# Optimization experiments

Measured on AMD Instinct MI355X. Metric: run time of the kernel, lower is better.

The kernel has to match this reference:

```python
import jax, jax.numpy as jnp
import numpy as np


def setup_inputs() -> dict:
    key = jax.random.key(0)
    kx, kw = jax.random.split(key)
    x = jax.random.normal(kx, (8192, 4096), dtype=jnp.float32)
    # weights initialized ~ N(0, 0.1) as in RandomNormal(stddev=0.1)
    w = jax.random.normal(kw, (4096, 4096), dtype=jnp.float32) * 0.1
    return {"x": x, "w": w}


def reference(x, w):
    # BinaryDense: sign-binarize both activations and weights, then matmul.
    x_bin = jnp.sign(x)  # [N, d_in], values in {-1, 0, +1}
    w_bin = jnp.sign(w)  # [d_in, units]
    return jnp.matmul(x_bin, w_bin)  # [N, units]
```

## Files before the change

### kernel.cpp

```cpp
#include <hip/hip_runtime.h>


#define M_DIM 8192
#define K_DIM 4096
#define N_DIM 4096
#define KB2   (K_DIM / 2)
#define HALFB 64
#define NH    (KB2 / HALFB)
#define HTILE (256 * HALFB)
#define SLOTB (2 * HTILE)

typedef int   v4i  __attribute__((ext_vector_type(4)));
typedef int   v8i  __attribute__((ext_vector_type(8)));
typedef float v16f __attribute__((ext_vector_type(16)));

__device__ __forceinline__ unsigned int nib4(float x) {
    return x > 0.0f ? 0x2u : (x < 0.0f ? 0xAu : 0x0u);
}

__global__ __launch_bounds__(256) void pack_both(const float* __restrict__ x,
                                                 unsigned short* __restrict__ xq,
                                                 const float* __restrict__ w,
                                                 unsigned char* __restrict__ wT) {
    if (blockIdx.x < 32768u) {
        size_t t = (size_t)blockIdx.x * 256 + threadIdx.x;
        float4 f = ((const float4*)x)[t];
        unsigned int v = nib4(f.x) | (nib4(f.y) << 4) | (nib4(f.z) << 8) | (nib4(f.w) << 12);
        xq[t] = (unsigned short)v;
        return;
    }
    __shared__ unsigned char sT[64][132];
    const unsigned id = blockIdx.x - 32768u;
    const int t  = threadIdx.x;
    const int n0 = (int)(id & 31) * 128;
    const int kb = (int)(id >> 5);
    const int k0 = kb * 64;

    const int cq = t & 31;
    const int r0 = t >> 5;
#pragma unroll
    for (int p = 0; p < 8; ++p) {
        int r = r0 + 8 * p;
        float4 f = *(const float4*)(w + (size_t)(k0 + r) * N_DIM + n0 + cq * 4);
        uchar4 c;
        c.x = (unsigned char)nib4(f.x);
        c.y = (unsigned char)nib4(f.y);
        c.z = (unsigned char)nib4(f.z);
        c.w = (unsigned char)nib4(f.w);
        *(uchar4*)(&sT[r][cq * 4]) = c;
    }
    __syncthreads();

    const int n  = t >> 1;
    const int kq = t & 1;
    union { unsigned char b[16]; int4 v; } u;
#pragma unroll
    for (int j = 0; j < 16; ++j) {
        unsigned lo = sT[kq * 32 + 2 * j][n];
        unsigned hi = sT[kq * 32 + 2 * j + 1][n];
        u.b[j] = (unsigned char)(lo | (hi << 4));
    }
    *(int4*)(wT + (size_t)(n0 + n) * KB2 + (size_t)kb * 32 + kq * 16) = u.v;
}

__device__ __forceinline__ v8i widen(v4i x) {
    v8i r;
    r[0] = x[0]; r[1] = x[1]; r[2] = x[2]; r[3] = x[3];
    r[4] = 0; r[5] = 0; r[6] = 0; r[7] = 0;
    return r;
}

__device__ __forceinline__ void gload16(const unsigned char* g, unsigned char* l) {
    __builtin_amdgcn_global_load_lds(
        (__attribute__((address_space(1))) void*)(void*)g,
        (__attribute__((address_space(3))) void*)l, 16, 0, 0);
}

__global__ __launch_bounds__(512, 2) void bgemm_fp4(const unsigned char* __restrict__ A,
                                                    const unsigned char* __restrict__ B,
                                                    float* __restrict__ C) {
    __shared__ __align__(16) unsigned char lds[4 * SLOTB];

    const int tid  = threadIdx.x;
    const int lane = tid & 63;
    const int wave = tid >> 6;
    const int wm   = wave >> 2;
    const int wn   = wave & 3;
    const int l31  = lane & 31;
    const int lhi  = lane >> 5;

    const int m0 = blockIdx.y * 256;
    const int n0 = blockIdx.x * 256;

    v16f acc[4][2] = {};

    const unsigned char* gAsrc[2];
    const unsigned char* gBsrc[2];
    int dstOff[2];
#pragma unroll
    for (int i = 0; i < 2; ++i) {
        int g   = i * 512 + tid;
        int q   = g >> 3;
        int t   = (g & 7) ^ (q & 7);
        int row = 2 * q + (t >> 2);
        int kc  = t & 3;
        gAsrc[i] = A + (size_t)(m0 + row) * KB2 + kc * 16;
        gBsrc[i] = B + (size_t)(n0 + row) * KB2 + kc * 16;
        dstOff[i] = g * 16;
    }

    int offA[2][4], offB[2][2];
#pragma unroll
    for (int ks = 0; ks < 2; ++ks) {
        const int kc = 2 * ks + lhi;
#pragma unroll
        for (int tm = 0; tm < 4; ++tm) {
            int r    = wm * 128 + tm * 32 + l31;
            int q    = r >> 1;
            int slot = (((r & 1) << 2) | kc) ^ (q & 7);
            offA[ks][tm] = q * 128 + slot * 16;
        }
#pragma unroll
        for (int tn = 0; tn < 2; ++tn) {
            int r    = wn * 64 + tn * 32 + l31;
            int q    = r >> 1;
            int slot = (((r & 1) << 2) | kc) ^ (q & 7);
            offB[ks][tn] = q * 128 + slot * 16;
        }
    }

    auto stage = [&](int h) {
        unsigned char* s = lds + (h & 3) * SLOTB;
        const size_t ko = (size_t)h * HALFB;
#pragma unroll
        for (int i = 0; i < 2; ++i) {
            gload16(gAsrc[i] + ko, s + dstOff[i]);
            gload16(gBsrc[i] + ko, s + HTILE + dstOff[i]);
        }
    };

    auto compute = [&](int h) {
        const unsigned char* sA = lds + (h & 3) * SLOTB;
        const unsigned char* sB = sA + HTILE;
#pragma unroll
        for (int ks = 0; ks < 2; ++ks) {
            v4i a4[4], b4[2];
#pragma unroll
            for (int tm = 0; tm < 4; ++tm) a4[tm] = *(const v4i*)(sA + offA[ks][tm]);
#pragma unroll
            for (int tn = 0; tn < 2; ++tn) b4[tn] = *(const v4i*)(sB + offB[ks][tn]);
            __builtin_amdgcn_s_setprio(1);
#pragma unroll
            for (int tm = 0; tm < 4; ++tm)
#pragma unroll
                for (int tn = 0; tn < 2; ++tn)
                    acc[tm][tn] = __builtin_amdgcn_mfma_scale_f32_32x32x64_f8f6f4(
                        widen(a4[tm]), widen(b4[tn]), acc[tm][tn],
                        4, 4,
                        0, 0x7F7F7F7F,
                        0, 0x7F7F7F7F);
            __builtin_amdgcn_s_setprio(0);
        }
    };

    stage(0); stage(1); stage(2);
    for (int h = 0; h < NH - 3; ++h) {
        asm volatile("s_waitcnt vmcnt(8)" ::: "memory");
        __builtin_amdgcn_s_barrier();
        stage(h + 3);
        compute(h);
    }
    asm volatile("s_waitcnt vmcnt(8)" ::: "memory");
    __builtin_amdgcn_s_barrier();
    compute(NH - 3);
    asm volatile("s_waitcnt vmcnt(4)" ::: "memory");
    __builtin_amdgcn_s_barrier();
    compute(NH - 2);
    asm volatile("s_waitcnt vmcnt(0)" ::: "memory");
    __builtin_amdgcn_s_barrier();
    compute(NH - 1);

#pragma unroll
    for (int tm = 0; tm < 4; ++tm) {
#pragma unroll
        for (int tn = 0; tn < 2; ++tn) {
            const int col  = n0 + wn * 64 + tn * 32 + l31;
            const int rowb = m0 + wm * 128 + tm * 32 + 4 * lhi;
#pragma unroll
            for (int r = 0; r < 16; ++r) {
                int row = rowb + (r & 3) + 8 * (r >> 2);
                __builtin_nontemporal_store(acc[tm][tn][r], &C[(size_t)row * N_DIM + col]);
            }
        }
    }
}

extern "C" void kernel_launch(void* const* d_in, const int* in_sizes, int n_in,
                              void* d_out, int out_size, void* d_ws, size_t ws_size,
                              hipStream_t stream) {
    const float* x = (const float*)d_in[0];
    const float* w = (const float*)d_in[1];
    float* out = (float*)d_out;

    unsigned char* xq = (unsigned char*)d_ws;
    unsigned char* wq = xq + (size_t)M_DIM * KB2;

    pack_both<<<dim3(32768 + 2048), dim3(256), 0, stream>>>(
        x, (unsigned short*)xq, w, wq);
    bgemm_fp4<<<dim3(N_DIM / 256, M_DIM / 256), dim3(512), 0, stream>>>(xq, wq, out);
}
```

Measured before the change: 324.6 us.

## Double-buffer LDS fragment reads across MFMAs and swizzle blocks per XCD

Restructures the main loop so LDS fragment loads for the next k-substep are issued while the current MFMA batch runs, using two register fragment sets, and moves the barrier to one per half-tile after staging. It also remaps a 1D grid so consecutive blocks on each XCD cover nearby output tiles, to improve L2 reuse of A/B. This costs extra registers for the second fragment set and a longer hand-unrolled epilogue.

After: 323.2 us. About the same (-0.5%).

```diff
diff --git a/kernel.cpp b/kernel.cpp
--- a/kernel.cpp
+++ b/kernel.cpp
@@ -76,6 +76,31 @@
         (__attribute__((address_space(3))) void*)l, 16, 0, 0);
 }
 
+#define RD_FRAGS(A4, B2, BASE, KS)                                   \
+    do {                                                             \
+        const unsigned char* sA_ = lds + (BASE);                     \
+        const unsigned char* sB_ = sA_ + HTILE;                      \
+        A4[0] = *(const v4i*)(sA_ + offA[KS][0]);                    \
+        A4[1] = *(const v4i*)(sA_ + offA[KS][1]);                    \
+        A4[2] = *(const v4i*)(sA_ + offA[KS][2]);                    \
+        A4[3] = *(const v4i*)(sA_ + offA[KS][3]);                    \
+        B2[0] = *(const v4i*)(sB_ + offB[KS][0]);                    \
+        B2[1] = *(const v4i*)(sB_ + offB[KS][1]);                    \
+    } while (0)
+
+#define MFMA8(A4, B2)                                                \
+    do {                                                             \
+        __builtin_amdgcn_s_setprio(1);                               \
+        _Pragma("unroll")                                            \
+        for (int tm_ = 0; tm_ < 4; ++tm_)                            \
+            _Pragma("unroll")                                        \
+            for (int tn_ = 0; tn_ < 2; ++tn_)                        \
+                acc[tm_][tn_] = __builtin_amdgcn_mfma_scale_f32_32x32x64_f8f6f4( \
+                    widen(A4[tm_]), widen(B2[tn_]), acc[tm_][tn_],   \
+                    4, 4, 0, 0x7F7F7F7F, 0, 0x7F7F7F7F);             \
+        __builtin_amdgcn_s_setprio(0);                               \
+    } while (0)
+
 __global__ __launch_bounds__(512, 2) void bgemm_fp4(const unsigned char* __restrict__ A,
                                                     const unsigned char* __restrict__ B,
                                                     float* __restrict__ C) {
@@ -89,8 +114,12 @@
     const int l31  = lane & 31;
     const int lhi  = lane >> 5;
 
-    const int m0 = blockIdx.y * 256;
-    const int n0 = blockIdx.x * 256;
+    const int id = (int)blockIdx.x;
+    const int sw = (id & 7) * 64 + (id >> 3);
+    const int bx = sw & 15;
+    const int by = sw >> 4;
+    const int m0 = by * 256;
+    const int n0 = bx * 256;
 
     v16f acc[4][2] = {};
 
@@ -139,46 +168,49 @@
         }
     };
 
-    auto compute = [&](int h) {
-        const unsigned char* sA = lds + (h & 3) * SLOTB;
-        const unsigned char* sB = sA + HTILE;
-#pragma unroll
-        for (int ks = 0; ks < 2; ++ks) {
-            v4i a4[4], b4[2];
-#pragma unroll
-            for (int tm = 0; tm < 4; ++tm) a4[tm] = *(const v4i*)(sA + offA[ks][tm]);
-#pragma unroll
-            for (int tn = 0; tn < 2; ++tn) b4[tn] = *(const v4i*)(sB + offB[ks][tn]);
-            __builtin_amdgcn_s_setprio(1);
-#pragma unroll
-            for (int tm = 0; tm < 4; ++tm)
-#pragma unroll
-                for (int tn = 0; tn < 2; ++tn)
-                    acc[tm][tn] = __builtin_amdgcn_mfma_scale_f32_32x32x64_f8f6f4(
-                        widen(a4[tm]), widen(b4[tn]), acc[tm][tn],
-                        4, 4,
-                        0, 0x7F7F7F7F,
-                        0, 0x7F7F7F7F);
-            __builtin_amdgcn_s_setprio(0);
-        }
-    };
+    v4i a0[4], b0[2];
+    v4i a1[4], b1[2];
 
     stage(0); stage(1); stage(2);
-    for (int h = 0; h < NH - 3; ++h) {
-        asm volatile("s_waitcnt vmcnt(8)" ::: "memory");
-        __builtin_amdgcn_s_barrier();
-        stage(h + 3);
-        compute(h);
-    }
-    asm volatile("s_waitcnt vmcnt(8)" ::: "memory");
-    __builtin_amdgcn_s_barrier();
-    compute(NH - 3);
     asm volatile("s_waitcnt vmcnt(4)" ::: "memory");
     __builtin_amdgcn_s_barrier();
-    compute(NH - 2);
-    asm volatile("s_waitcnt vmcnt(0)" ::: "memory");
-    __builtin_amdgcn_s_barrier();
-    compute(NH - 1);
+    RD_FRAGS(a0, b0, 0, 0);
+
+    for (int h = 0; h < NH - 3; ++h) {
+        const int sh  = (h & 3) * SLOTB;
+        const int sh1 = ((h + 1) & 3) * SLOTB;
+        RD_FRAGS(a1, b1, sh, 1);
+        MFMA8(a0, b0);
+        RD_FRAGS(a0, b0, sh1, 0);
+        stage(h + 3);
+        MFMA8(a1, b1);
+        asm volatile("s_waitcnt vmcnt(4)" ::: "memory");
+        __builtin_amdgcn_s_barrier();
+    }
+    {
+        const int sh  = ((NH - 3) & 3) * SLOTB;
+        const int sh1 = ((NH - 2) & 3) * SLOTB;
+        RD_FRAGS(a1, b1, sh, 1);
+        MFMA8(a0, b0);
+        RD_FRAGS(a0, b0, sh1, 0);
+        MFMA8(a1, b1);
+        asm volatile("s_waitcnt vmcnt(0)" ::: "memory");
+        __builtin_amdgcn_s_barrier();
+    }
+    {
+        const int sh  = ((NH - 2) & 3) * SLOTB;
+        const int sh1 = ((NH - 1) & 3) * SLOTB;
+        RD_FRAGS(a1, b1, sh, 1);
+        MFMA8(a0, b0);
+        RD_FRAGS(a0, b0, sh1, 0);
+        MFMA8(a1, b1);
+    }
+    {
+        const int sh = ((NH - 1) & 3) * SLOTB;
+        RD_FRAGS(a1, b1, sh, 1);
+        MFMA8(a0, b0);
+        MFMA8(a1, b1);
+    }
 
 #pragma unroll
     for (int tm = 0; tm < 4; ++tm) {
@@ -207,5 +239,5 @@
 
     pack_both<<<dim3(32768 + 2048), dim3(256), 0, stream>>>(
         x, (unsigned short*)xq, w, wq);
-    bgemm_fp4<<<dim3(N_DIM / 256, M_DIM / 256), dim3(512), 0, stream>>>(xq, wq, out);
-}
+    bgemm_fp4<<<dim3((M_DIM / 256) * (N_DIM / 256)), dim3(512), 0, stream>>>(xq, wq, out);
+}
```

## Load A fragments directly to registers with MFMA-ready pre-permuted packing

Applied to the files above, without the earlier changes.

The x-packing pass now writes activations in a layout that matches the MFMA lane pattern, so each wave can load its A operands straight from global memory into double-buffered registers without going through LDS. Only B stays staged in LDS, which halves LDS traffic and slot size. A 1D grid with an XCD-aware block swizzle is also added to improve L2 locality. The cost is more live registers and A loads that are no longer shared across waves, which can increase global/L2 traffic for the duplicated A reads.

Result: slower. 338.5 us (+4.3%).

```diff
diff --git a/kernel.cpp b/kernel.cpp
--- a/kernel.cpp
+++ b/kernel.cpp
@@ -7,8 +7,7 @@
 #define KB2   (K_DIM / 2)
 #define HALFB 64
 #define NH    (KB2 / HALFB)
-#define HTILE (256 * HALFB)
-#define SLOTB (2 * HTILE)
+#define SLOTB (256 * HALFB)
 
 typedef int   v4i  __attribute__((ext_vector_type(4)));
 typedef int   v8i  __attribute__((ext_vector_type(8)));
@@ -23,10 +22,16 @@
                                                  const float* __restrict__ w,
                                                  unsigned char* __restrict__ wT) {
     if (blockIdx.x < 32768u) {
-        size_t t = (size_t)blockIdx.x * 256 + threadIdx.x;
-        float4 f = ((const float4*)x)[t];
-        unsigned int v = nib4(f.x) | (nib4(f.y) << 4) | (nib4(f.z) << 8) | (nib4(f.w) << 12);
-        xq[t] = (unsigned short)v;
+        unsigned d   = blockIdx.x * 256 + threadIdx.x;
+        unsigned r5  = d >> 15;
+        unsigned h   = (d >> 10) & 31;
+        unsigned kc  = (d >> 8) & 3;
+        unsigned l31 = (d >> 3) & 31;
+        unsigned b2  = d & 7;
+        size_t   m   = (size_t)r5 * 32 + l31;
+        float4 f = ((const float4*)x)[m * 1024 + h * 32 + kc * 8 + b2];
+        unsigned v = nib4(f.x) | (nib4(f.y) << 4) | (nib4(f.z) << 8) | (nib4(f.w) << 12);
+        xq[d] = (unsigned short)v;
         return;
     }
     __shared__ unsigned char sT[64][132];
@@ -76,6 +81,35 @@
         (__attribute__((address_space(3))) void*)l, 16, 0, 0);
 }
 
+#define CLUSTER(AU, KS, BB)                                              \
+    do {                                                                 \
+        __builtin_amdgcn_s_setprio(1);                                   \
+        _Pragma("unroll")                                                \
+        for (int tm_ = 0; tm_ < 4; ++tm_)                                \
+            _Pragma("unroll")                                            \
+            for (int tn_ = 0; tn_ < 2; ++tn_)                            \
+                acc[tm_][tn_] = __builtin_amdgcn_mfma_scale_f32_32x32x64_f8f6f4( \
+                    widen(AU[(KS) * 4 + tm_]), widen(BB[tn_]), acc[tm_][tn_],    \
+                    4, 4, 0, 0x7F7F7F7F, 0, 0x7F7F7F7F);                 \
+        __builtin_amdgcn_s_setprio(0);                                   \
+    } while (0)
+
+#define BODY(H, AU, AF, DOA, DOS, VMC, DOBAR)                            \
+    do {                                                                 \
+        const unsigned char* sB_ = lds + ((H) & 3) * SLOTB;              \
+        v4i bb0_[2], bb1_[2];                                            \
+        bb0_[0] = *(const v4i*)(sB_ + offB[0][0]);                       \
+        bb0_[1] = *(const v4i*)(sB_ + offB[0][1]);                       \
+        if (DOA) loadA(AF, (H) + 1);                                     \
+        if (DOS) stageB((H) + 3);                                        \
+        CLUSTER(AU, 0, bb0_);                                            \
+        bb1_[0] = *(const v4i*)(sB_ + offB[1][0]);                       \
+        bb1_[1] = *(const v4i*)(sB_ + offB[1][1]);                       \
+        CLUSTER(AU, 1, bb1_);                                            \
+        asm volatile("s_waitcnt vmcnt(" #VMC ")" ::: "memory");          \
+        if (DOBAR) __builtin_amdgcn_s_barrier();                         \
+    } while (0)
+
 __global__ __launch_bounds__(512, 2) void bgemm_fp4(const unsigned char* __restrict__ A,
                                                     const unsigned char* __restrict__ B,
                                                     float* __restrict__ C) {
@@ -89,12 +123,14 @@
     const int l31  = lane & 31;
     const int lhi  = lane >> 5;
 
-    const int m0 = blockIdx.y * 256;
-    const int n0 = blockIdx.x * 256;
+    const int id = (int)blockIdx.x;
+    const int sw = (id & 7) * 64 + (id >> 3);
+    const int bx = sw & 15;
+    const int by = sw >> 4;
+    const int n0 = bx * 256;
 
     v16f acc[4][2] = {};
 
-    const unsigned char* gAsrc[2];
     const unsigned char* gBsrc[2];
     int dstOff[2];
 #pragma unroll
@@ -104,22 +140,14 @@
         int t   = (g & 7) ^ (q & 7);
         int row = 2 * q + (t >> 2);
         int kc  = t & 3;
-        gAsrc[i] = A + (size_t)(m0 + row) * KB2 + kc * 16;
         gBsrc[i] = B + (size_t)(n0 + row) * KB2 + kc * 16;
         dstOff[i] = g * 16;
     }
 
-    int offA[2][4], offB[2][2];
+    int offB[2][2];
 #pragma unroll
     for (int ks = 0; ks < 2; ++ks) {
         const int kc = 2 * ks + lhi;
-#pragma unroll
-        for (int tm = 0; tm < 4; ++tm) {
-            int r    = wm * 128 + tm * 32 + l31;
-            int q    = r >> 1;
-            int slot = (((r & 1) << 2) | kc) ^ (q & 7);
-            offA[ks][tm] = q * 128 + slot * 16;
-        }
 #pragma unroll
         for (int tn = 0; tn < 2; ++tn) {
             int r    = wn * 64 + tn * 32 + l31;
@@ -129,57 +157,43 @@
         }
     }
 
-    auto stage = [&](int h) {
+    const unsigned char* gA[4];
+#pragma unroll
+    for (int tm = 0; tm < 4; ++tm)
+        gA[tm] = A + ((size_t)(by * 8 + wm * 4 + tm) << 16) + lhi * 512 + l31 * 16;
+
+    auto stageB = [&](int h) {
         unsigned char* s = lds + (h & 3) * SLOTB;
         const size_t ko = (size_t)h * HALFB;
-#pragma unroll
-        for (int i = 0; i < 2; ++i) {
-            gload16(gAsrc[i] + ko, s + dstOff[i]);
-            gload16(gBsrc[i] + ko, s + HTILE + dstOff[i]);
+        gload16(gBsrc[0] + ko, s + dstOff[0]);
+        gload16(gBsrc[1] + ko, s + dstOff[1]);
+    };
+
+    v4i aA[8], aB[8];
+    auto loadA = [&](v4i (&R)[8], int h) {
+#pragma unroll
+        for (int tm = 0; tm < 4; ++tm) {
+            R[tm]     = *(const v4i*)(gA[tm] + (size_t)h * 2048);
+            R[4 + tm] = *(const v4i*)(gA[tm] + (size_t)h * 2048 + 1024);
         }
     };
 
-    auto compute = [&](int h) {
-        const unsigned char* sA = lds + (h & 3) * SLOTB;
-        const unsigned char* sB = sA + HTILE;
-#pragma unroll
-        for (int ks = 0; ks < 2; ++ks) {
-            v4i a4[4], b4[2];
-#pragma unroll
-            for (int tm = 0; tm < 4; ++tm) a4[tm] = *(const v4i*)(sA + offA[ks][tm]);
-#pragma unroll
-            for (int tn = 0; tn < 2; ++tn) b4[tn] = *(const v4i*)(sB + offB[ks][tn]);
-            __builtin_amdgcn_s_setprio(1);
-#pragma unroll
-            for (int tm = 0; tm < 4; ++tm)
-#pragma unroll
-                for (int tn = 0; tn < 2; ++tn)
-                    acc[tm][tn] = __builtin_amdgcn_mfma_scale_f32_32x32x64_f8f6f4(
-                        widen(a4[tm]), widen(b4[tn]), acc[tm][tn],
-                        4, 4,
-                        0, 0x7F7F7F7F,
-                        0, 0x7F7F7F7F);
-            __builtin_amdgcn_s_setprio(0);
-        }
-    };
-
-    stage(0); stage(1); stage(2);
-    for (int h = 0; h < NH - 3; ++h) {
-        asm volatile("s_waitcnt vmcnt(8)" ::: "memory");
-        __builtin_amdgcn_s_barrier();
-        stage(h + 3);
-        compute(h);
-    }
-    asm volatile("s_waitcnt vmcnt(8)" ::: "memory");
+    stageB(0); stageB(1); stageB(2);
+    loadA(aA, 0);
+    asm volatile("s_waitcnt vmcnt(12)" ::: "memory");
     __builtin_amdgcn_s_barrier();
-    compute(NH - 3);
-    asm volatile("s_waitcnt vmcnt(4)" ::: "memory");
-    __builtin_amdgcn_s_barrier();
-    compute(NH - 2);
-    asm volatile("s_waitcnt vmcnt(0)" ::: "memory");
-    __builtin_amdgcn_s_barrier();
-    compute(NH - 1);
-
+
+#pragma unroll 1
+    for (int h = 0; h < NH - 4; h += 2) {
+        BODY(h,     aA, aB, 1, 1, 12, 1);
+        BODY(h + 1, aB, aA, 1, 1, 12, 1);
+    }
+    BODY(28, aA, aB, 1, 1, 12, 1);
+    BODY(29, aB, aA, 1, 0, 10, 1);
+    BODY(30, aA, aB, 1, 0, 8, 1);
+    BODY(31, aB, aA, 0, 0, 0, 0);
+
+    const int m0 = by * 256;
 #pragma unroll
     for (int tm = 0; tm < 4; ++tm) {
 #pragma unroll
@@ -207,5 +221,5 @@
 
     pack_both<<<dim3(32768 + 2048), dim3(256), 0, stream>>>(
         x, (unsigned short*)xq, w, wq);
-    bgemm_fp4<<<dim3(N_DIM / 256, M_DIM / 256), dim3(512), 0, stream>>>(xq, wq, out);
-}
+    bgemm_fp4<<<dim3((M_DIM / 256) * (N_DIM / 256)), dim3(512), 0, stream>>>(xq, wq, out);
+}
```

## Interleave global-to-LDS loads with per-substep MFMA phases and swizzle block order

Applied to the files above, without the earlier changes.

Each K half-tile's compute is split into two phases. Each phase reads its LDS fragments, issues half of the next stage's global-to-LDS loads, synchronizes, and then runs its MFMAs, so loads are spread more evenly across the MFMA work. The launch grid becomes 1D, with block IDs remapped so that consecutive blocks are spread over the tile grid, which is meant to target L2 locality and XCD distribution. The change adds barriers per phase, which could increase synchronization stalls.

Result: no change. 325.4 us (+0.2%).

```diff
diff --git a/kernel.cpp b/kernel.cpp
--- a/kernel.cpp
+++ b/kernel.cpp
@@ -7,8 +7,8 @@
 #define KB2   (K_DIM / 2)
 #define HALFB 64
 #define NH    (KB2 / HALFB)
-#define HTILE (256 * HALFB)
-#define SLOTB (2 * HTILE)
+#define ATILE (256 * HALFB)
+#define SLOTB (2 * ATILE)
 
 typedef int   v4i  __attribute__((ext_vector_type(4)));
 typedef int   v8i  __attribute__((ext_vector_type(8)));
@@ -76,6 +76,39 @@
         (__attribute__((address_space(3))) void*)l, 16, 0, 0);
 }
 
+#define PHASE(H, KS, DOS, DOW, VMC, DOBAR)                               \
+    do {                                                                 \
+        const unsigned char* sA_ = lds + ((H) & 3) * SLOTB;              \
+        const unsigned char* sB_ = sA_ + ATILE;                          \
+        v4i a_[4], b_[2];                                                \
+        a_[0] = *(const v4i*)(sA_ + offA[KS][0]);                        \
+        a_[1] = *(const v4i*)(sA_ + offA[KS][1]);                        \
+        a_[2] = *(const v4i*)(sA_ + offA[KS][2]);                        \
+        a_[3] = *(const v4i*)(sA_ + offA[KS][3]);                        \
+        b_[0] = *(const v4i*)(sB_ + offB[KS][0]);                        \
+        b_[1] = *(const v4i*)(sB_ + offB[KS][1]);                        \
+        if (DOS) {                                                       \
+            unsigned char* st_ = lds + (((H) + 3) & 3) * SLOTB;          \
+            const size_t ko_ = (size_t)((H) + 3) * HALFB;                \
+            gload16(gAsrc[KS] + ko_, st_ + dstOff[KS]);                  \
+            gload16(gBsrc[KS] + ko_, st_ + ATILE + dstOff[KS]);          \
+        }                                                                \
+        __builtin_amdgcn_s_barrier();                                    \
+        asm volatile("s_waitcnt lgkmcnt(0)" ::: "memory");               \
+        __builtin_amdgcn_sched_barrier(0);                               \
+        __builtin_amdgcn_s_setprio(1);                                   \
+        _Pragma("unroll")                                                \
+        for (int tm_ = 0; tm_ < 4; ++tm_)                                \
+            _Pragma("unroll")                                            \
+            for (int tn_ = 0; tn_ < 2; ++tn_)                            \
+                acc[tm_][tn_] = __builtin_amdgcn_mfma_scale_f32_32x32x64_f8f6f4( \
+                    widen(a_[tm_]), widen(b_[tn_]), acc[tm_][tn_],       \
+                    4, 4, 0, 0x7F7F7F7F, 0, 0x7F7F7F7F);                 \
+        __builtin_amdgcn_s_setprio(0);                                   \
+        if (DOW) asm volatile("s_waitcnt vmcnt(" #VMC ")" ::: "memory"); \
+        if (DOBAR) __builtin_amdgcn_s_barrier();                         \
+    } while (0)
+
 __global__ __launch_bounds__(512, 2) void bgemm_fp4(const unsigned char* __restrict__ A,
                                                     const unsigned char* __restrict__ B,
                                                     float* __restrict__ C) {
@@ -89,8 +122,12 @@
     const int l31  = lane & 31;
     const int lhi  = lane >> 5;
 
-    const int m0 = blockIdx.y * 256;
-    const int n0 = blockIdx.x * 256;
+    const int id = (int)blockIdx.x;
+    const int sw = (id & 7) * 64 + (id >> 3);
+    const int bx = sw & 15;
+    const int by = sw >> 4;
+    const int m0 = by * 256;
+    const int n0 = bx * 256;
 
     v16f acc[4][2] = {};
 
@@ -129,56 +166,31 @@
         }
     }
 
-    auto stage = [&](int h) {
+    auto stage_full = [&](int h) {
         unsigned char* s = lds + (h & 3) * SLOTB;
         const size_t ko = (size_t)h * HALFB;
 #pragma unroll
         for (int i = 0; i < 2; ++i) {
             gload16(gAsrc[i] + ko, s + dstOff[i]);
-            gload16(gBsrc[i] + ko, s + HTILE + dstOff[i]);
+            gload16(gBsrc[i] + ko, s + ATILE + dstOff[i]);
         }
     };
 
-    auto compute = [&](int h) {
-        const unsigned char* sA = lds + (h & 3) * SLOTB;
-        const unsigned char* sB = sA + HTILE;
-#pragma unroll
-        for (int ks = 0; ks < 2; ++ks) {
-            v4i a4[4], b4[2];
-#pragma unroll
-            for (int tm = 0; tm < 4; ++tm) a4[tm] = *(const v4i*)(sA + offA[ks][tm]);
-#pragma unroll
-            for (int tn = 0; tn < 2; ++tn) b4[tn] = *(const v4i*)(sB + offB[ks][tn]);
-            __builtin_amdgcn_s_setprio(1);
-#pragma unroll
-            for (int tm = 0; tm < 4; ++tm)
-#pragma unroll
-                for (int tn = 0; tn < 2; ++tn)
-                    acc[tm][tn] = __builtin_amdgcn_mfma_scale_f32_32x32x64_f8f6f4(
-                        widen(a4[tm]), widen(b4[tn]), acc[tm][tn],
-                        4, 4,
-                        0, 0x7F7F7F7F,
-                        0, 0x7F7F7F7F);
-            __builtin_amdgcn_s_setprio(0);
-        }
-    };
-
-    stage(0); stage(1); stage(2);
-    for (int h = 0; h < NH - 3; ++h) {
-        asm volatile("s_waitcnt vmcnt(8)" ::: "memory");
-        __builtin_amdgcn_s_barrier();
-        stage(h + 3);
-        compute(h);
-    }
+    stage_full(0); stage_full(1); stage_full(2);
     asm volatile("s_waitcnt vmcnt(8)" ::: "memory");
     __builtin_amdgcn_s_barrier();
-    compute(NH - 3);
-    asm volatile("s_waitcnt vmcnt(4)" ::: "memory");
-    __builtin_amdgcn_s_barrier();
-    compute(NH - 2);
-    asm volatile("s_waitcnt vmcnt(0)" ::: "memory");
-    __builtin_amdgcn_s_barrier();
-    compute(NH - 1);
+
+#pragma unroll 1
+    for (int h = 0; h < NH - 3; ++h) {
+        PHASE(h, 0, 1, 0, 0, 1);
+        PHASE(h, 1, 1, 1, 8, 1);
+    }
+    PHASE(NH - 3, 0, 0, 0, 0, 1);
+    PHASE(NH - 3, 1, 0, 1, 4, 1);
+    PHASE(NH - 2, 0, 0, 0, 0, 1);
+    PHASE(NH - 2, 1, 0, 1, 0, 1);
+    PHASE(NH - 1, 0, 0, 0, 0, 1);
+    PHASE(NH - 1, 1, 0, 0, 0, 0);
 
 #pragma unroll
     for (int tm = 0; tm < 4; ++tm) {
@@ -207,5 +219,5 @@
 
     pack_both<<<dim3(32768 + 2048), dim3(256), 0, stream>>>(
         x, (unsigned short*)xq, w, wq);
-    bgemm_fp4<<<dim3(N_DIM / 256, M_DIM / 256), dim3(512), 0, stream>>>(xq, wq, out);
-}
+    bgemm_fp4<<<dim3((M_DIM / 256) * (N_DIM / 256)), dim3(512), 0, stream>>>(xq, wq, out);
+}
```
